# Kernel optimization log

Hardware: AMD Instinct MI355X
Metric: run time of the kernel (lower is better)

The kernel has to match this reference:

```python
import jax, jax.numpy as jnp
import numpy as np

TEMPERATURE = 8.0  # sqrt(d_head=64)


def setup_inputs() -> dict:
    key = jax.random.key(0)
    kq, kk, kv, km = jax.random.split(key, 4)
    B, N, L, D = 2, 16, 2048, 64
    q = jax.random.normal(kq, (B, N, L, D), dtype=jnp.float32)
    k = jax.random.normal(kk, (B, N, L, D), dtype=jnp.float32)
    v = jax.random.normal(kv, (B, N, L, D), dtype=jnp.float32)
    mask = jax.random.randint(km, (B, N, L, L), 0, 2).astype(jnp.bool_)
    return {"q": q, "k": k, "v": v, "mask": mask}


def reference(q, k, v, mask):
    # attn = (q @ k^T) / temperature, shape [b, n, lq, lk]
    attn = jnp.einsum("bnqd,bnkd->bnqk", q, k) / TEMPERATURE
    attn = jnp.where(mask, -jnp.inf, attn)
    attn = jax.nn.softmax(attn, axis=-1)
    attn = jnp.where(mask, 0.0, attn)
    # dropout is identity in eval/reference mode
    output = jnp.einsum("bnqk,bnkd->bnqd", attn, v)
    return (output, attn)
```

## Files before the change

### kernel.cpp

```cpp
#include <hip/hip_runtime.h>
#include <math.h>

#define L 2048
#define D 64
#define MT 32
#define KT 128
#define NT 256

typedef short bf16x8 __attribute__((ext_vector_type(8)));
typedef short bf16x4 __attribute__((ext_vector_type(4)));
typedef float f32x4  __attribute__((ext_vector_type(4)));

#define MFMA16 __builtin_amdgcn_mfma_f32_16x16x32_bf16

__device__ __forceinline__ short f2bf(float f) {
    union { float f; unsigned u; } x; x.f = f;
    unsigned r = x.u + 0x7fffu + ((x.u >> 16) & 1u);
    return (short)(r >> 16);
}

__global__ __launch_bounds__(NT) void conv_swz(
    const float* __restrict__ src, short* __restrict__ dst, int nrows)
{
    int g = blockIdx.x * NT + threadIdx.x;
    if (g >= nrows * 8) return;
    int row = g >> 3, c = g & 7;
    const float4* s4 = (const float4*)(src + (size_t)row * D + c * 8);
    float4 a = s4[0], b = s4[1];
    bf16x8 t;
    t[0]=f2bf(a.x); t[1]=f2bf(a.y); t[2]=f2bf(a.z); t[3]=f2bf(a.w);
    t[4]=f2bf(b.x); t[5]=f2bf(b.y); t[6]=f2bf(b.z); t[7]=f2bf(b.w);
    *(bf16x8*)(dst + (size_t)row * D + ((c ^ (row & 7)) * 8)) = t;
}

__global__ __launch_bounds__(NT) void vtrans(
    const float* __restrict__ v, short* __restrict__ vt)
{
    const int h  = blockIdx.x >> 4;
    const int kt = blockIdx.x & 15;
    const float* src = v + ((size_t)h * L + (size_t)kt * KT) * D;
    short* dst = vt + (size_t)blockIdx.x * (D * KT);
    __shared__ short Vs[KT * 68];
    const int t = threadIdx.x;
    {
        const int r = t & 127, seg = t >> 7;
        const float4* s4 = (const float4*)(src + r * D + seg * 32);
        #pragma unroll
        for (int kq = 0; kq < 8; ++kq) {
            float4 a = s4[kq];
            bf16x4 b;
            b[0]=f2bf(a.x); b[1]=f2bf(a.y); b[2]=f2bf(a.z); b[3]=f2bf(a.w);
            *(bf16x4*)(Vs + r * 68 + seg * 32 + kq * 4) = b;
        }
    }
    __syncthreads();
    #pragma unroll
    for (int j = 0; j < 4; ++j) {
        const int cg = t + NT * j;
        const int d = cg >> 4, c = cg & 15;
        bf16x8 o;
        #pragma unroll
        for (int jj = 0; jj < 8; ++jj) o[jj] = Vs[(c * 8 + jj) * 68 + d];
        *(bf16x8*)(dst + d * KT + ((c ^ (d & 7)) * 8)) = o;
    }
}

__global__ __launch_bounds__(NT, 4) void sdpa_fused(
    const short* __restrict__ qb,
    const short* __restrict__ kb,
    const short* __restrict__ vtb,
    const int*   __restrict__ mask,
    float* __restrict__ out,
    float* __restrict__ attn,
    float* __restrict__ invs)
{
    const int bid  = blockIdx.x;
    const int bn   = bid >> 6;
    const int qt   = bid & 63;
    const int row0 = qt * MT;
    const int tid  = threadIdx.x;
    const int wave = tid >> 6;
    const int lane = tid & 63;
    const int lq   = lane & 15;
    const int lg   = lane >> 4;
    const int swz  = lq & 7;

    __shared__ __align__(16) char smem[40960];
    short* Kb = (short*)smem;
    short* Vb = (short*)(smem + 16384);
    short* Ps = (short*)(smem + 32768);
    short* Qt = Ps;
    float* sums_w = (float*)(smem + 32768);
    float* inv_l  = (float*)(smem + 32768 + 512);

    const short* qh = qb  + (size_t)bn * L * D;
    const short* kh = kb  + (size_t)bn * L * D;
    const int*   mg = mask + ((size_t)bn * L + row0) * L;
    float*       ag = attn + ((size_t)bn * L + row0) * L;

    *(bf16x8*)(Qt + tid * 8) = *(const bf16x8*)(qh + (size_t)row0 * D + tid * 8);
    __syncthreads();
    bf16x8 qf[2][2];
    #pragma unroll
    for (int qq = 0; qq < 2; ++qq)
        #pragma unroll
        for (int s = 0; s < 2; ++s)
            qf[qq][s] = *(const bf16x8*)(Qt + (qq*16 + lq) * D + (((s*4 + lg) ^ swz) * 8));
    __syncthreads();

    f32x4 of[2] = {};
    float sumreg[2] = {0.f, 0.f};

    for (int kt = 0; kt < L / KT; ++kt) {
        const int kb0 = kt * KT;
        const short* ks = kh + (size_t)kb0 * D;
        const short* vs = vtb + ((size_t)bn * (L / KT) + kt) * (D * KT);
        bf16x8 kr[4], vr[4];
        #pragma unroll
        for (int c = 0; c < 4; ++c) {
            kr[c] = *(const bf16x8*)(ks + (c * NT + tid) * 8);
            vr[c] = *(const bf16x8*)(vs + (c * NT + tid) * 8);
        }
        int4 m4[2][2];
        #pragma unroll
        for (int kk = 0; kk < 2; ++kk)
            #pragma unroll
            for (int qq = 0; qq < 2; ++qq)
                m4[kk][qq] = *(const int4*)(mg + (size_t)(qq*16 + lq) * L
                                               + kb0 + wave*32 + kk*16 + lg*4);
        __syncthreads();
        #pragma unroll
        for (int c = 0; c < 4; ++c) {
            *(bf16x8*)(Kb + (c * NT + tid) * 8) = kr[c];
            *(bf16x8*)(Vb + (c * NT + tid) * 8) = vr[c];
        }
        __syncthreads();

        f32x4 acc[2][2] = {};
        __builtin_amdgcn_s_setprio(1);
        #pragma unroll
        for (int s = 0; s < 2; ++s) {
            bf16x8 a0 = *(const bf16x8*)(Kb + (wave*32 + lq)      * D + (((s*4 + lg) ^ swz) * 8));
            bf16x8 a1 = *(const bf16x8*)(Kb + (wave*32 + 16 + lq) * D + (((s*4 + lg) ^ swz) * 8));
            acc[0][0] = MFMA16(a0, qf[0][s], acc[0][0], 0, 0, 0);
            acc[0][1] = MFMA16(a0, qf[1][s], acc[0][1], 0, 0, 0);
            acc[1][0] = MFMA16(a1, qf[0][s], acc[1][0], 0, 0, 0);
            acc[1][1] = MFMA16(a1, qf[1][s], acc[1][1], 0, 0, 0);
        }
        __builtin_amdgcn_s_setprio(0);

        #pragma unroll
        for (int kk = 0; kk < 2; ++kk)
            #pragma unroll
            for (int qq = 0; qq < 2; ++qq) {
                const int qrow = qq*16 + lq;
                const int colL = wave*32 + kk*16 + lg*4;
                const int4 m = m4[kk][qq];
                const f32x4 a = acc[kk][qq];
                const float e0 = m.x ? 0.f : __expf(a[0] * 0.125f);
                const float e1 = m.y ? 0.f : __expf(a[1] * 0.125f);
                const float e2 = m.z ? 0.f : __expf(a[2] * 0.125f);
                const float e3 = m.w ? 0.f : __expf(a[3] * 0.125f);
                sumreg[qq] += (e0 + e1) + (e2 + e3);
                float4 ev; ev.x = e0; ev.y = e1; ev.z = e2; ev.w = e3;
                *(float4*)(ag + (size_t)qrow * L + kb0 + colL) = ev;
                bf16x4 pb;
                pb[0]=f2bf(e0); pb[1]=f2bf(e1); pb[2]=f2bf(e2); pb[3]=f2bf(e3);
                *(bf16x4*)(Ps + qrow * KT + (colL ^ (swz * 8))) = pb;
            }
        __syncthreads();

        __builtin_amdgcn_s_setprio(1);
        #pragma unroll
        for (int s2 = 0; s2 < 4; ++s2) {
            const int ch = ((s2*4 + lg) ^ swz) * 8;
            bf16x8 vb = *(const bf16x8*)(Vb + (wave*16 + lq) * KT + ch);
            bf16x8 p0 = *(const bf16x8*)(Ps + lq * KT + ch);
            bf16x8 p1 = *(const bf16x8*)(Ps + (16 + lq) * KT + ch);
            of[0] = MFMA16(p0, vb, of[0], 0, 0, 0);
            of[1] = MFMA16(p1, vb, of[1], 0, 0, 0);
        }
        __builtin_amdgcn_s_setprio(0);
    }

    #pragma unroll
    for (int qq = 0; qq < 2; ++qq) {
        sumreg[qq] += __shfl_xor(sumreg[qq], 16, 64);
        sumreg[qq] += __shfl_xor(sumreg[qq], 32, 64);
    }
    __syncthreads();
    if (lane < 16) {
        sums_w[wave * 32 + lq]      = sumreg[0];
        sums_w[wave * 32 + 16 + lq] = sumreg[1];
    }
    __syncthreads();
    if (tid < MT) {
        const float s = sums_w[tid] + sums_w[32 + tid] + sums_w[64 + tid] + sums_w[96 + tid];
        const float inv = 1.0f / s;
        inv_l[tid] = inv;
        invs[(size_t)bn * L + row0 + tid] = inv;
    }
    __syncthreads();
    #pragma unroll
    for (int r = 0; r < 2; ++r)
        #pragma unroll
        for (int i = 0; i < 4; ++i) {
            const int qrow = r*16 + lg*4 + i;
            out[((size_t)bn * L + row0 + qrow) * D + wave*16 + lq] = of[r][i] * inv_l[qrow];
        }
}

__global__ __launch_bounds__(NT) void scale_attn(
    float* __restrict__ attn, const float* __restrict__ invs, long long total4)
{
    long long i = (long long)blockIdx.x * NT + threadIdx.x;
    const long long stride = (long long)gridDim.x * NT;
    float4* a4 = (float4*)attn;
    for (; i < total4; i += stride) {
        const float inv = invs[i >> 9];
        float4 t = a4[i];
        t.x *= inv; t.y *= inv; t.z *= inv; t.w *= inv;
        a4[i] = t;
    }
}

extern "C" void kernel_launch(void* const* d_in, const int* in_sizes, int n_in,
                              void* d_out, int out_size, void* d_ws, size_t ws_size,
                              hipStream_t stream) {
    const float* q    = (const float*)d_in[0];
    const float* k    = (const float*)d_in[1];
    const float* v    = (const float*)d_in[2];
    const int*   mask = (const int*)d_in[3];

    float* out = (float*)d_out;
    const int rows = in_sizes[0] / D;
    float* attn = out + (size_t)rows * D;

    short* qb   = (short*)d_ws;
    short* kb   = qb  + (size_t)rows * D;
    short* vtb  = kb  + (size_t)rows * D;
    float* invs = (float*)(vtb + (size_t)rows * D);

    const int heads = rows / L;
    conv_swz<<<rows * 8 / NT, NT, 0, stream>>>(q, qb, rows);
    conv_swz<<<rows * 8 / NT, NT, 0, stream>>>(k, kb, rows);
    vtrans<<<heads * (L / KT), NT, 0, stream>>>(v, vtb);
    sdpa_fused<<<rows / MT, NT, 0, stream>>>(qb, kb, vtb, mask, out, attn, invs);
    scale_attn<<<8192, NT, 0, stream>>>(attn, invs, (long long)rows * (L / 4));
}
```

Measured before the change: 1.193 ms.

## Fuse attn normalization into main kernel via fp16 scratch in output rows

Switches bf16 to fp16 MFMA, doubles the query tile to 64 rows with 512 threads, and fuses the Q conversion into the main kernel. Unnormalized exponentials are stored as fp16 in the first half of each attn row, then read back and rescaled in place, which removes the separate scale_attn pass. K, V and mask loads are now register-prefetched one tile ahead, and block IDs are remapped. The in-place scratch reuse depends on barrier ordering within the final loop, and fp16 precision replaces bf16.

```diff
diff --git a/kernel.cpp b/kernel.cpp
--- a/kernel.cpp
+++ b/kernel.cpp
@@ -3,44 +3,40 @@
 
 #define L 2048
 #define D 64
-#define MT 32
+#define MT 64
 #define KT 128
-#define NT 256
-
-typedef short bf16x8 __attribute__((ext_vector_type(8)));
-typedef short bf16x4 __attribute__((ext_vector_type(4)));
+#define NT 512
+#define CNT 256
+#define NTILE (L / KT)
+
+typedef _Float16 halfx8 __attribute__((ext_vector_type(8)));
+typedef _Float16 halfx4 __attribute__((ext_vector_type(4)));
 typedef float f32x4  __attribute__((ext_vector_type(4)));
 
-#define MFMA16 __builtin_amdgcn_mfma_f32_16x16x32_bf16
-
-__device__ __forceinline__ short f2bf(float f) {
-    union { float f; unsigned u; } x; x.f = f;
-    unsigned r = x.u + 0x7fffu + ((x.u >> 16) & 1u);
-    return (short)(r >> 16);
-}
-
-__global__ __launch_bounds__(NT) void conv_swz(
-    const float* __restrict__ src, short* __restrict__ dst, int nrows)
+#define MFMA16 __builtin_amdgcn_mfma_f32_16x16x32_f16
+
+__global__ __launch_bounds__(CNT) void conv_swz(
+    const float* __restrict__ src, _Float16* __restrict__ dst, int nrows)
 {
-    int g = blockIdx.x * NT + threadIdx.x;
+    int g = blockIdx.x * CNT + threadIdx.x;
     if (g >= nrows * 8) return;
     int row = g >> 3, c = g & 7;
     const float4* s4 = (const float4*)(src + (size_t)row * D + c * 8);
     float4 a = s4[0], b = s4[1];
-    bf16x8 t;
-    t[0]=f2bf(a.x); t[1]=f2bf(a.y); t[2]=f2bf(a.z); t[3]=f2bf(a.w);
-    t[4]=f2bf(b.x); t[5]=f2bf(b.y); t[6]=f2bf(b.z); t[7]=f2bf(b.w);
-    *(bf16x8*)(dst + (size_t)row * D + ((c ^ (row & 7)) * 8)) = t;
-}
-
-__global__ __launch_bounds__(NT) void vtrans(
-    const float* __restrict__ v, short* __restrict__ vt)
+    halfx8 t;
+    t[0]=(_Float16)a.x; t[1]=(_Float16)a.y; t[2]=(_Float16)a.z; t[3]=(_Float16)a.w;
+    t[4]=(_Float16)b.x; t[5]=(_Float16)b.y; t[6]=(_Float16)b.z; t[7]=(_Float16)b.w;
+    *(halfx8*)(dst + (size_t)row * D + ((c ^ (row & 7)) * 8)) = t;
+}
+
+__global__ __launch_bounds__(CNT) void vtrans(
+    const float* __restrict__ v, _Float16* __restrict__ vt)
 {
     const int h  = blockIdx.x >> 4;
     const int kt = blockIdx.x & 15;
     const float* src = v + ((size_t)h * L + (size_t)kt * KT) * D;
-    short* dst = vt + (size_t)blockIdx.x * (D * KT);
-    __shared__ short Vs[KT * 68];
+    _Float16* dst = vt + (size_t)blockIdx.x * (D * KT);
+    __shared__ _Float16 Vs[KT * 68];
     const int t = threadIdx.x;
     {
         const int r = t & 127, seg = t >> 7;
@@ -48,35 +44,35 @@
         #pragma unroll
         for (int kq = 0; kq < 8; ++kq) {
             float4 a = s4[kq];
-            bf16x4 b;
-            b[0]=f2bf(a.x); b[1]=f2bf(a.y); b[2]=f2bf(a.z); b[3]=f2bf(a.w);
-            *(bf16x4*)(Vs + r * 68 + seg * 32 + kq * 4) = b;
+            halfx4 b;
+            b[0]=(_Float16)a.x; b[1]=(_Float16)a.y; b[2]=(_Float16)a.z; b[3]=(_Float16)a.w;
+            *(halfx4*)(Vs + r * 68 + seg * 32 + kq * 4) = b;
         }
     }
     __syncthreads();
     #pragma unroll
     for (int j = 0; j < 4; ++j) {
-        const int cg = t + NT * j;
+        const int cg = t + CNT * j;
         const int d = cg >> 4, c = cg & 15;
-        bf16x8 o;
+        halfx8 o;
         #pragma unroll
         for (int jj = 0; jj < 8; ++jj) o[jj] = Vs[(c * 8 + jj) * 68 + d];
-        *(bf16x8*)(dst + d * KT + ((c ^ (d & 7)) * 8)) = o;
-    }
-}
-
-__global__ __launch_bounds__(NT, 4) void sdpa_fused(
-    const short* __restrict__ qb,
-    const short* __restrict__ kb,
-    const short* __restrict__ vtb,
-    const int*   __restrict__ mask,
+        *(halfx8*)(dst + d * KT + ((c ^ (d & 7)) * 8)) = o;
+    }
+}
+
+__global__ __launch_bounds__(NT, 6) void sdpa_fused(
+    const _Float16* __restrict__ kb,
+    const _Float16* __restrict__ vtb,
+    const float*    __restrict__ q,
+    const int*      __restrict__ mask,
     float* __restrict__ out,
-    float* __restrict__ attn,
-    float* __restrict__ invs)
+    float* __restrict__ attn)
 {
-    const int bid  = blockIdx.x;
-    const int bn   = bid >> 6;
-    const int qt   = bid & 63;
+    const int bid0 = blockIdx.x;
+    const int bid  = (bid0 & 7) * 128 + (bid0 >> 3);
+    const int bn   = bid >> 5;
+    const int qt   = bid & 31;
     const int row0 = qt * MT;
     const int tid  = threadIdx.x;
     const int wave = tid >> 6;
@@ -85,98 +81,114 @@
     const int lg   = lane >> 4;
     const int swz  = lq & 7;
 
-    __shared__ __align__(16) char smem[40960];
-    short* Kb = (short*)smem;
-    short* Vb = (short*)(smem + 16384);
-    short* Ps = (short*)(smem + 32768);
-    short* Qt = Ps;
+    __shared__ __align__(16) char smem[49152];
+    _Float16* Kb = (_Float16*)smem;
+    _Float16* Vb = (_Float16*)(smem + 16384);
+    _Float16* Ps = (_Float16*)(smem + 32768);
+    _Float16* Qt = Ps;
     float* sums_w = (float*)(smem + 32768);
-    float* inv_l  = (float*)(smem + 32768 + 512);
-
-    const short* qh = qb  + (size_t)bn * L * D;
-    const short* kh = kb  + (size_t)bn * L * D;
-    const int*   mg = mask + ((size_t)bn * L + row0) * L;
-    float*       ag = attn + ((size_t)bn * L + row0) * L;
-
-    *(bf16x8*)(Qt + tid * 8) = *(const bf16x8*)(qh + (size_t)row0 * D + tid * 8);
-    __syncthreads();
-    bf16x8 qf[2][2];
-    #pragma unroll
-    for (int qq = 0; qq < 2; ++qq)
+    float* inv_l  = (float*)(smem + 32768 + 2048);
+
+    const _Float16* kh = kb  + (size_t)bn * (L * D);
+    const _Float16* vh = vtb + (size_t)bn * (L * D);
+    const int*      mg = mask + ((size_t)bn * L + row0) * L;
+    float*          ag = attn + ((size_t)bn * L + row0) * L;
+    _Float16*       eh = (_Float16*)ag;
+
+    {
+        const int r = tid >> 3, c = tid & 7;
+        const float4* s4 = (const float4*)(q + ((size_t)bn * L + row0 + r) * D + c * 8);
+        float4 a = s4[0], b = s4[1];
+        halfx8 t;
+        t[0]=(_Float16)a.x; t[1]=(_Float16)a.y; t[2]=(_Float16)a.z; t[3]=(_Float16)a.w;
+        t[4]=(_Float16)b.x; t[5]=(_Float16)b.y; t[6]=(_Float16)b.z; t[7]=(_Float16)b.w;
+        *(halfx8*)(Qt + r * D + ((c ^ (r & 7)) * 8)) = t;
+    }
+    __syncthreads();
+    halfx8 qf[4][2];
+    #pragma unroll
+    for (int qq = 0; qq < 4; ++qq)
         #pragma unroll
         for (int s = 0; s < 2; ++s)
-            qf[qq][s] = *(const bf16x8*)(Qt + (qq*16 + lq) * D + (((s*4 + lg) ^ swz) * 8));
+            qf[qq][s] = *(const halfx8*)(Qt + (qq*16 + lq) * D + (((s*4 + lg) ^ swz) * 8));
     __syncthreads();
 
     f32x4 of[2] = {};
-    float sumreg[2] = {0.f, 0.f};
-
-    for (int kt = 0; kt < L / KT; ++kt) {
-        const int kb0 = kt * KT;
-        const short* ks = kh + (size_t)kb0 * D;
-        const short* vs = vtb + ((size_t)bn * (L / KT) + kt) * (D * KT);
-        bf16x8 kr[4], vr[4];
-        #pragma unroll
-        for (int c = 0; c < 4; ++c) {
-            kr[c] = *(const bf16x8*)(ks + (c * NT + tid) * 8);
-            vr[c] = *(const bf16x8*)(vs + (c * NT + tid) * 8);
-        }
-        int4 m4[2][2];
-        #pragma unroll
-        for (int kk = 0; kk < 2; ++kk)
+    float sumreg[4] = {0.f, 0.f, 0.f, 0.f};
+
+    halfx8 kr0 = *(const halfx8*)(kh + tid * 8);
+    halfx8 kr1 = *(const halfx8*)(kh + (NT + tid) * 8);
+    halfx8 vr0 = *(const halfx8*)(vh + tid * 8);
+    halfx8 vr1 = *(const halfx8*)(vh + (NT + tid) * 8);
+    int4 m4[4], m4n[4];
+    #pragma unroll
+    for (int qq = 0; qq < 4; ++qq)
+        m4[qq] = *(const int4*)(mg + (size_t)(qq*16 + lq) * L + wave*16 + lg*4);
+
+    #pragma unroll 2
+    for (int t = 0; t < NTILE; ++t) {
+        const int kb0 = t * KT;
+        __syncthreads();
+        *(halfx8*)(Kb + tid * 8)        = kr0;
+        *(halfx8*)(Kb + (NT + tid) * 8) = kr1;
+        *(halfx8*)(Vb + tid * 8)        = vr0;
+        *(halfx8*)(Vb + (NT + tid) * 8) = vr1;
+        __syncthreads();
+        if (t + 1 < NTILE) {
+            const _Float16* ks = kh + (size_t)(kb0 + KT) * D;
+            const _Float16* vs = vh + (size_t)(t + 1) * (KT * D);
+            kr0 = *(const halfx8*)(ks + tid * 8);
+            kr1 = *(const halfx8*)(ks + (NT + tid) * 8);
+            vr0 = *(const halfx8*)(vs + tid * 8);
+            vr1 = *(const halfx8*)(vs + (NT + tid) * 8);
             #pragma unroll
-            for (int qq = 0; qq < 2; ++qq)
-                m4[kk][qq] = *(const int4*)(mg + (size_t)(qq*16 + lq) * L
-                                               + kb0 + wave*32 + kk*16 + lg*4);
-        __syncthreads();
-        #pragma unroll
-        for (int c = 0; c < 4; ++c) {
-            *(bf16x8*)(Kb + (c * NT + tid) * 8) = kr[c];
-            *(bf16x8*)(Vb + (c * NT + tid) * 8) = vr[c];
-        }
-        __syncthreads();
-
-        f32x4 acc[2][2] = {};
+            for (int qq = 0; qq < 4; ++qq)
+                m4n[qq] = *(const int4*)(mg + (size_t)(qq*16 + lq) * L
+                                            + (kb0 + KT) + wave*16 + lg*4);
+        }
+
+        f32x4 acc[4] = {};
         __builtin_amdgcn_s_setprio(1);
         #pragma unroll
         for (int s = 0; s < 2; ++s) {
-            bf16x8 a0 = *(const bf16x8*)(Kb + (wave*32 + lq)      * D + (((s*4 + lg) ^ swz) * 8));
-            bf16x8 a1 = *(const bf16x8*)(Kb + (wave*32 + 16 + lq) * D + (((s*4 + lg) ^ swz) * 8));
-            acc[0][0] = MFMA16(a0, qf[0][s], acc[0][0], 0, 0, 0);
-            acc[0][1] = MFMA16(a0, qf[1][s], acc[0][1], 0, 0, 0);
-            acc[1][0] = MFMA16(a1, qf[0][s], acc[1][0], 0, 0, 0);
-            acc[1][1] = MFMA16(a1, qf[1][s], acc[1][1], 0, 0, 0);
+            halfx8 a = *(const halfx8*)(Kb + (wave*16 + lq) * D + (((s*4 + lg) ^ swz) * 8));
+            acc[0] = MFMA16(a, qf[0][s], acc[0], 0, 0, 0);
+            acc[1] = MFMA16(a, qf[1][s], acc[1], 0, 0, 0);
+            acc[2] = MFMA16(a, qf[2][s], acc[2], 0, 0, 0);
+            acc[3] = MFMA16(a, qf[3][s], acc[3], 0, 0, 0);
         }
         __builtin_amdgcn_s_setprio(0);
 
-        #pragma unroll
-        for (int kk = 0; kk < 2; ++kk)
+        const int colL = wave*16 + lg*4;
+        #pragma unroll
+        for (int qq = 0; qq < 4; ++qq) {
+            const int qrow = qq*16 + lq;
+            const int4 m = m4[qq];
+            const f32x4 a = acc[qq];
+            const float e0 = m.x ? 0.f : __expf(a[0] * 0.125f);
+            const float e1 = m.y ? 0.f : __expf(a[1] * 0.125f);
+            const float e2 = m.z ? 0.f : __expf(a[2] * 0.125f);
+            const float e3 = m.w ? 0.f : __expf(a[3] * 0.125f);
+            sumreg[qq] += (e0 + e1) + (e2 + e3);
+            halfx4 pb;
+            pb[0]=(_Float16)e0; pb[1]=(_Float16)e1; pb[2]=(_Float16)e2; pb[3]=(_Float16)e3;
+            *(halfx4*)(eh + (size_t)qrow * (2*L) + kb0 + colL) = pb;
+            *(halfx4*)(Ps + qrow * KT + (colL ^ (swz << 3))) = pb;
+        }
+        if (t + 1 < NTILE) {
             #pragma unroll
-            for (int qq = 0; qq < 2; ++qq) {
-                const int qrow = qq*16 + lq;
-                const int colL = wave*32 + kk*16 + lg*4;
-                const int4 m = m4[kk][qq];
-                const f32x4 a = acc[kk][qq];
-                const float e0 = m.x ? 0.f : __expf(a[0] * 0.125f);
-                const float e1 = m.y ? 0.f : __expf(a[1] * 0.125f);
-                const float e2 = m.z ? 0.f : __expf(a[2] * 0.125f);
-                const float e3 = m.w ? 0.f : __expf(a[3] * 0.125f);
-                sumreg[qq] += (e0 + e1) + (e2 + e3);
-                float4 ev; ev.x = e0; ev.y = e1; ev.z = e2; ev.w = e3;
-                *(float4*)(ag + (size_t)qrow * L + kb0 + colL) = ev;
-                bf16x4 pb;
-                pb[0]=f2bf(e0); pb[1]=f2bf(e1); pb[2]=f2bf(e2); pb[3]=f2bf(e3);
-                *(bf16x4*)(Ps + qrow * KT + (colL ^ (swz * 8))) = pb;
-            }
-        __syncthreads();
-
+            for (int qq = 0; qq < 4; ++qq) m4[qq] = m4n[qq];
+        }
+        __syncthreads();
+
+        const int wr = wave >> 2, wc = wave & 3;
         __builtin_amdgcn_s_setprio(1);
         #pragma unroll
         for (int s2 = 0; s2 < 4; ++s2) {
             const int ch = ((s2*4 + lg) ^ swz) * 8;
-            bf16x8 vb = *(const bf16x8*)(Vb + (wave*16 + lq) * KT + ch);
-            bf16x8 p0 = *(const bf16x8*)(Ps + lq * KT + ch);
-            bf16x8 p1 = *(const bf16x8*)(Ps + (16 + lq) * KT + ch);
+            halfx8 vb = *(const halfx8*)(Vb + (wc*16 + lq) * KT + ch);
+            halfx8 p0 = *(const halfx8*)(Ps + (wr*32 + lq) * KT + ch);
+            halfx8 p1 = *(const halfx8*)(Ps + (wr*32 + 16 + lq) * KT + ch);
             of[0] = MFMA16(p0, vb, of[0], 0, 0, 0);
             of[1] = MFMA16(p1, vb, of[1], 0, 0, 0);
         }
@@ -184,43 +196,50 @@
     }
 
     #pragma unroll
-    for (int qq = 0; qq < 2; ++qq) {
+    for (int qq = 0; qq < 4; ++qq) {
         sumreg[qq] += __shfl_xor(sumreg[qq], 16, 64);
         sumreg[qq] += __shfl_xor(sumreg[qq], 32, 64);
     }
     __syncthreads();
     if (lane < 16) {
-        sums_w[wave * 32 + lq]      = sumreg[0];
-        sums_w[wave * 32 + 16 + lq] = sumreg[1];
+        #pragma unroll
+        for (int qq = 0; qq < 4; ++qq)
+            sums_w[wave * 64 + qq*16 + lane] = sumreg[qq];
     }
     __syncthreads();
     if (tid < MT) {
-        const float s = sums_w[tid] + sums_w[32 + tid] + sums_w[64 + tid] + sums_w[96 + tid];
-        const float inv = 1.0f / s;
-        inv_l[tid] = inv;
-        invs[(size_t)bn * L + row0 + tid] = inv;
-    }
-    __syncthreads();
-    #pragma unroll
-    for (int r = 0; r < 2; ++r)
-        #pragma unroll
-        for (int i = 0; i < 4; ++i) {
-            const int qrow = r*16 + lg*4 + i;
-            out[((size_t)bn * L + row0 + qrow) * D + wave*16 + lq] = of[r][i] * inv_l[qrow];
-        }
-}
-
-__global__ __launch_bounds__(NT) void scale_attn(
-    float* __restrict__ attn, const float* __restrict__ invs, long long total4)
-{
-    long long i = (long long)blockIdx.x * NT + threadIdx.x;
-    const long long stride = (long long)gridDim.x * NT;
-    float4* a4 = (float4*)attn;
-    for (; i < total4; i += stride) {
-        const float inv = invs[i >> 9];
-        float4 t = a4[i];
-        t.x *= inv; t.y *= inv; t.z *= inv; t.w *= inv;
-        a4[i] = t;
+        float s = 0.f;
+        #pragma unroll
+        for (int w = 0; w < 8; ++w) s += sums_w[w * 64 + tid];
+        inv_l[tid] = 1.0f / s;
+    }
+    __syncthreads();
+
+    {
+        const int wr = wave >> 2, wc = wave & 3;
+        #pragma unroll
+        for (int r = 0; r < 2; ++r)
+            #pragma unroll
+            for (int i = 0; i < 4; ++i) {
+                const int qrow = wr*32 + r*16 + lg*4 + i;
+                out[((size_t)bn * L + row0 + qrow) * D + wc*16 + lq] = of[r][i] * inv_l[qrow];
+            }
+    }
+
+    #pragma unroll 1
+    for (int p = 0; p < 32; ++p) {
+        const int rr = p*2 + (tid >> 8);
+        const int c0 = (tid & 255) * 8;
+        halfx8 ev = *(const halfx8*)(eh + (size_t)rr * (2*L) + c0);
+        const float inv = inv_l[rr];
+        __syncthreads();
+        float4 o0, o1;
+        o0.x = (float)ev[0] * inv; o0.y = (float)ev[1] * inv;
+        o0.z = (float)ev[2] * inv; o0.w = (float)ev[3] * inv;
+        o1.x = (float)ev[4] * inv; o1.y = (float)ev[5] * inv;
+        o1.z = (float)ev[6] * inv; o1.w = (float)ev[7] * inv;
+        *(float4*)(ag + (size_t)rr * L + c0)     = o0;
+        *(float4*)(ag + (size_t)rr * L + c0 + 4) = o1;
     }
 }
 
@@ -236,15 +255,10 @@
     const int rows = in_sizes[0] / D;
     float* attn = out + (size_t)rows * D;
 
-    short* qb   = (short*)d_ws;
-    short* kb   = qb  + (size_t)rows * D;
-    short* vtb  = kb  + (size_t)rows * D;
-    float* invs = (float*)(vtb + (size_t)rows * D);
-
-    const int heads = rows / L;
-    conv_swz<<<rows * 8 / NT, NT, 0, stream>>>(q, qb, rows);
-    conv_swz<<<rows * 8 / NT, NT, 0, stream>>>(k, kb, rows);
-    vtrans<<<heads * (L / KT), NT, 0, stream>>>(v, vtb);
-    sdpa_fused<<<rows / MT, NT, 0, stream>>>(qb, kb, vtb, mask, out, attn, invs);
-    scale_attn<<<8192, NT, 0, stream>>>(attn, invs, (long long)rows * (L / 4));
-}
+    _Float16* kbuf = (_Float16*)d_ws;
+    _Float16* vtb  = kbuf + (size_t)rows * D;
+
+    conv_swz<<<rows * 8 / CNT, CNT, 0, stream>>>(k, kbuf, rows);
+    vtrans<<<(rows / L) * NTILE, CNT, 0, stream>>>(v, vtb);
+    sdpa_fused<<<rows / MT, NT, 0, stream>>>(kbuf, vtb, q, mask, out, attn);
+}
```

Measured after the change: 1.702 ms. +42.7%, slower.
